# Performance work log

Measured on AMD Instinct MI355X. Metric: run time of the kernel, lower is better.

Reference implementation:

```python
import jax, jax.numpy as jnp
import numpy as np
from jax.ops import segment_sum

N_NODES = 100000
N_EDGES = 1600000
IN_DIM = 64
NUM_GRAPHS = 64
BN_EPS = 1e-5


def setup_inputs() -> dict:
    key = jax.random.key(0)
    ks = jax.random.split(key, 32)
    inp = {
        "x": jax.random.normal(ks[0], (N_NODES, IN_DIM), jnp.float32),
        "edge_index": jax.random.randint(ks[1], (2, N_EDGES), 0, N_NODES, jnp.int64),
        "edge_weight": jax.random.uniform(ks[2], (N_EDGES,), jnp.float32),
        "batch": jnp.sort(jax.random.randint(ks[3], (N_NODES,), 0, NUM_GRAPHS, jnp.int64)),
    }
    dims = [(IN_DIM, 32), (32, 64), (64, 128)]
    i = 4
    for li, (din, dout) in enumerate(dims, start=1):
        inp[f"w{li}"] = jax.random.normal(ks[i], (din, dout), jnp.float32) / np.sqrt(din); i += 1
        inp[f"b{li}"] = jax.random.normal(ks[i], (dout,), jnp.float32) * 0.01; i += 1
        inp[f"g{li}"] = 1.0 + 0.1 * jax.random.normal(ks[i], (dout,), jnp.float32); i += 1
        inp[f"be{li}"] = jax.random.normal(ks[i], (dout,), jnp.float32) * 0.01; i += 1
        inp[f"m{li}"] = jax.random.normal(ks[i], (dout,), jnp.float32) * 0.1; i += 1
        inp[f"v{li}"] = jax.random.uniform(ks[i], (dout,), jnp.float32) + 0.5; i += 1
    inp["fcw"] = jax.random.normal(ks[i], (128, 64), jnp.float32) / np.sqrt(128.0); i += 1
    inp["fcb"] = jax.random.normal(ks[i], (64,), jnp.float32) * 0.01; i += 1
    inp["ow"] = jax.random.normal(ks[i], (64, 1), jnp.float32) / 8.0; i += 1
    inp["ob"] = jax.random.normal(ks[i], (1,), jnp.float32) * 0.01
    return inp


def _gcn_norm(edge_index, edge_weight, n):
    # PyG GCNConv: add self-loops (weight 1), symmetric normalization.
    row, col = edge_index[0], edge_index[1]
    deg = segment_sum(edge_weight, col, num_segments=n) + 1.0  # +1 from self-loop
    dinv = jnp.where(deg > 0, 1.0 / jnp.sqrt(deg), 0.0)
    norm = dinv[row] * edge_weight * dinv[col]   # [E]
    self_norm = dinv * dinv                      # [N], self-loop coefficient
    return norm, self_norm


def _conv(x, w, b, row, col, norm, self_norm, n):
    h = x @ w                                                       # [N, dout]
    agg = segment_sum(h[row] * norm[:, None], col, num_segments=n)  # gather-scale-scatter
    return agg + self_norm[:, None] * h + b


def _bn_relu(x, g, be, m, v):
    # BatchNorm1d in eval mode (running stats), fused with ReLU. Dropout = identity (eval).
    return jax.nn.relu((x - m) * (g / jnp.sqrt(v + BN_EPS)) + be)


def reference(x, edge_index, edge_weight, batch,
              w1, b1, g1, be1, m1, v1,
              w2, b2, g2, be2, m2, v2,
              w3, b3, g3, be3, m3, v3,
              fcw, fcb, ow, ob):
    n = x.shape[0]
    row, col = edge_index[0], edge_index[1]
    norm, self_norm = _gcn_norm(edge_index, edge_weight, n)

    h = _bn_relu(_conv(x, w1, b1, row, col, norm, self_norm, n), g1, be1, m1, v1)
    h = _bn_relu(_conv(h, w2, b2, row, col, norm, self_norm, n), g2, be2, m2, v2)
    h = _bn_relu(_conv(h, w3, b3, row, col, norm, self_norm, n), g3, be3, m3, v3)

    # global mean pool over graphs
    sums = segment_sum(h, batch, num_segments=NUM_GRAPHS)                       # [G,128]
    cnts = segment_sum(jnp.ones((n,), h.dtype), batch, num_segments=NUM_GRAPHS)
    pooled = sums / jnp.maximum(cnts, 1.0)[:, None]

    h = jax.nn.relu(pooled @ fcw + fcb)
    return h @ ow + ob
```

## Files before the change

kernel.cpp:

```cpp
#include <hip/hip_runtime.h>
#include <math.h>

#define BN_EPS 1e-5f
#define NBSH 7
#define BKT 128

__device__ __forceinline__ float4 fma4(float s, float4 a, float4 b) {
    return make_float4(fmaf(s, a.x, b.x), fmaf(s, a.y, b.y),
                       fmaf(s, a.z, b.z), fmaf(s, a.w, b.w));
}
__device__ __forceinline__ float4 add4(float4 a, float4 b) {
    return make_float4(a.x + b.x, a.y + b.y, a.z + b.z, a.w + b.w);
}


__global__ __launch_bounds__(256) void chist_k(const int* __restrict__ ei,
                                               int* __restrict__ chist, int E, int NB) {
    __shared__ int h[1024];
    int t = threadIdx.x;
    for (int i = t; i < NB; i += 256) h[i] = 0;
    __syncthreads();
    for (int e = blockIdx.x * 256 + t; e < E; e += gridDim.x * 256)
        atomicAdd(&h[((unsigned)ei[E + e]) >> NBSH], 1);
    __syncthreads();
    for (int i = t; i < NB; i += 256) if (h[i]) atomicAdd(&chist[i], h[i]);
}

__global__ __launch_bounds__(1024) void cscan_k(const int* __restrict__ chist,
                                                int* __restrict__ cbase,
                                                int* __restrict__ ccur,
                                                int NB, int* __restrict__ rptrN, int E) {
    __shared__ int s[1024];
    int t = threadIdx.x;
    int v = (t < NB) ? chist[t] : 0;
    s[t] = v;
    __syncthreads();
    for (int off = 1; off < 1024; off <<= 1) {
        int x = (t >= off) ? s[t - off] : 0;
        __syncthreads();
        s[t] += x;
        __syncthreads();
    }
    int excl = s[t] - v;
    if (t < NB) { cbase[t] = excl; ccur[t] = excl; }
    if (t == 0) { cbase[NB] = E; rptrN[0] = E; }
}

__global__ __launch_bounds__(256) void cscat_k(const int* __restrict__ ei,
                                               const float* __restrict__ ew,
                                               int* __restrict__ ccur,
                                               int2* __restrict__ pairs0, int E, int NB) {
    __shared__ int h[1024];
    __shared__ int base[1024];
    int t = threadIdx.x;
    int CH = (E + gridDim.x - 1) / gridDim.x;
    int lo = blockIdx.x * CH;
    int hi = lo + CH < E ? lo + CH : E;

    for (int i = t; i < NB; i += 256) h[i] = 0;
    __syncthreads();
    for (int e = lo + t; e < hi; e += 256)
        atomicAdd(&h[((unsigned)ei[E + e]) >> NBSH], 1);
    __syncthreads();
    for (int i = t; i < NB; i += 256) {
        int c = h[i];
        base[i] = c ? atomicAdd(&ccur[i], c) : 0;
        h[i] = 0;
    }
    __syncthreads();
    for (int e = lo + t; e < hi; e += 256) {
        int c = ei[E + e];
        int b = ((unsigned)c) >> NBSH;
        int idx = base[b] + atomicAdd(&h[b], 1);
        pairs0[idx] = make_int2(ei[e] | ((c & (BKT - 1)) << 17), __float_as_int(ew[e]));
    }
}

__global__ __launch_bounds__(BKT) void fineA_k(const int2* __restrict__ pairs0,
                                               const int* __restrict__ cbase,
                                               int* __restrict__ rptr,
                                               float* __restrict__ dinv, int N) {
    int b = blockIdx.x;
    __shared__ int cnt[BKT];
    __shared__ float wsum[BKT];
    __shared__ int sc[BKT];
    int t = threadIdx.x;
    cnt[t] = 0; wsum[t] = 0.f;
    __syncthreads();
    int s = cbase[b], e = cbase[b + 1];
    for (int i = s + t; i < e; i += BKT) {
        int2 p = pairs0[i];
        int cib = ((unsigned)p.x) >> 17;
        atomicAdd(&cnt[cib], 1);
        atomicAdd(&wsum[cib], __int_as_float(p.y));
    }
    __syncthreads();
    int v = cnt[t];
    sc[t] = v;
    __syncthreads();
    for (int off = 1; off < BKT; off <<= 1) {
        int x = (t >= off) ? sc[t - off] : 0;
        __syncthreads();
        sc[t] += x;
        __syncthreads();
    }
    int node = b * BKT + t;
    if (node < N) {
        rptr[node] = s + sc[t] - v;
        dinv[node] = 1.0f / sqrtf(wsum[t] + 1.0f);
    }
}

__global__ __launch_bounds__(BKT) void fineB_k(const int2* __restrict__ pairs0,
                                               const int* __restrict__ cbase,
                                               const int* __restrict__ rptr,
                                               const float* __restrict__ dinv,
                                               int2* __restrict__ pairs, int N) {
    int b = blockIdx.x;
    __shared__ int cur[BKT];
    __shared__ float dc[BKT];
    int t = threadIdx.x;
    int node = b * BKT + t;
    cur[t] = (node < N) ? rptr[node] : 0;
    dc[t] = (node < N) ? dinv[node] : 0.f;
    __syncthreads();
    int s = cbase[b], e = cbase[b + 1];
    for (int i = s + t; i < e; i += BKT) {
        int2 p = pairs0[i];
        int cib = ((unsigned)p.x) >> 17;
        int row = p.x & 0x1FFFF;
        float nw = dinv[row] * __int_as_float(p.y) * dc[cib];
        int pos = atomicAdd(&cur[cib], 1);
        pairs[pos] = make_int2(row, __float_as_int(nw));
    }
}

template <int DIN, int DOUT>
__global__ __launch_bounds__(256) void matmul_k(const float* __restrict__ x,
                                                const float* __restrict__ w,
                                                float* __restrict__ h, int n) {
    constexpr int RPB = 64;
    constexpr int XS = DIN + 4;
    constexpr int J = DOUT / 16;
    __shared__ float xs[RPB * XS];
    __shared__ float4 ws4[DIN * (DOUT / 4)];
    int t = threadIdx.x;
    int row0 = blockIdx.x * RPB;

    for (int i = t; i < DIN * DOUT / 4; i += 256) ws4[i] = ((const float4*)w)[i];
    for (int i = t; i < RPB * DIN / 4; i += 256) {
        int r = i / (DIN / 4), kq = i % (DIN / 4);
        int gr = row0 + r;
        float4 xv = (gr < n) ? ((const float4*)x)[(size_t)gr * (DIN / 4) + kq]
                             : make_float4(0.f, 0.f, 0.f, 0.f);
        *(float4*)&xs[r * XS + kq * 4] = xv;
    }
    __syncthreads();

    int r = t >> 2, cg = t & 3;
    float4 acc[J];
#pragma unroll
    for (int j = 0; j < J; ++j) acc[j] = make_float4(0.f, 0.f, 0.f, 0.f);

    for (int k = 0; k < DIN; ++k) {
        float xv = xs[r * XS + k];
#pragma unroll
        for (int j = 0; j < J; ++j) {
            float4 wv = ws4[k * (DOUT / 4) + cg + 4 * j];
            acc[j] = fma4(xv, wv, acc[j]);
        }
    }
    int gr = row0 + r;
    if (gr < n) {
#pragma unroll
        for (int j = 0; j < J; ++j)
            ((float4*)h)[(size_t)gr * (DOUT / 4) + cg + 4 * j] = acc[j];
    }
}

template <int DIN, int DOUT>
__global__ __launch_bounds__(256) void matmulBN_k(const float* __restrict__ x,
                                                  const float* __restrict__ w,
                                                  const float* __restrict__ bias,
                                                  const float* __restrict__ g,
                                                  const float* __restrict__ be,
                                                  const float* __restrict__ m,
                                                  const float* __restrict__ v,
                                                  float* __restrict__ h, int n) {
    constexpr int RPB = 64;
    constexpr int XS = DIN + 4;
    constexpr int J = DOUT / 16;
    __shared__ float xs[RPB * XS];
    __shared__ float4 ws4[DIN * (DOUT / 4)];
    int t = threadIdx.x;
    int row0 = blockIdx.x * RPB;

    for (int i = t; i < DIN * DOUT / 4; i += 256) ws4[i] = ((const float4*)w)[i];
    for (int i = t; i < RPB * DIN / 4; i += 256) {
        int r = i / (DIN / 4), kq = i % (DIN / 4);
        int gr = row0 + r;
        float4 xv = (gr < n) ? ((const float4*)x)[(size_t)gr * (DIN / 4) + kq]
                             : make_float4(0.f, 0.f, 0.f, 0.f);
        *(float4*)&xs[r * XS + kq * 4] = xv;
    }
    __syncthreads();

    int r = t >> 2, cg = t & 3;
    float4 acc[J];
#pragma unroll
    for (int j = 0; j < J; ++j) acc[j] = make_float4(0.f, 0.f, 0.f, 0.f);

    for (int k = 0; k < DIN; ++k) {
        float xv = xs[r * XS + k];
#pragma unroll
        for (int j = 0; j < J; ++j) {
            float4 wv = ws4[k * (DOUT / 4) + cg + 4 * j];
            acc[j] = fma4(xv, wv, acc[j]);
        }
    }
    int gr = row0 + r;
    if (gr < n) {
#pragma unroll
        for (int j = 0; j < J; ++j) {
            int c4 = cg + 4 * j;
            float4 bb = ((const float4*)bias)[c4];
            float4 gg = ((const float4*)g)[c4];
            float4 ee = ((const float4*)be)[c4];
            float4 mm = ((const float4*)m)[c4];
            float4 vv = ((const float4*)v)[c4];
            float4 o = acc[j];
            float4 res;
            res.x = fmaxf((o.x + bb.x - mm.x) * (gg.x / sqrtf(vv.x + BN_EPS)) + ee.x, 0.f);
            res.y = fmaxf((o.y + bb.y - mm.y) * (gg.y / sqrtf(vv.y + BN_EPS)) + ee.y, 0.f);
            res.z = fmaxf((o.z + bb.z - mm.z) * (gg.z / sqrtf(vv.z + BN_EPS)) + ee.z, 0.f);
            res.w = fmaxf((o.w + bb.w - mm.w) * (gg.w / sqrtf(vv.w + BN_EPS)) + ee.w, 0.f);
            ((float4*)h)[(size_t)gr * (DOUT / 4) + c4] = res;
        }
    }
}

template <int TPN>
__device__ __forceinline__ float4 gather4(const float* __restrict__ h,
                                          const int2* __restrict__ pairs,
                                          int s, int e, int lc) {
    float4 a0 = make_float4(0.f, 0.f, 0.f, 0.f);
    float4 a1 = a0, a2 = a0, a3 = a0;
    int i = s;
    for (; i + 4 <= e; i += 4) {
        int2 p0 = pairs[i + 0];
        int2 p1 = pairs[i + 1];
        int2 p2 = pairs[i + 2];
        int2 p3 = pairs[i + 3];
        float4 h0 = ((const float4*)h)[(size_t)p0.x * TPN + lc];
        float4 h1 = ((const float4*)h)[(size_t)p1.x * TPN + lc];
        float4 h2 = ((const float4*)h)[(size_t)p2.x * TPN + lc];
        float4 h3 = ((const float4*)h)[(size_t)p3.x * TPN + lc];
        a0 = fma4(__int_as_float(p0.y), h0, a0);
        a1 = fma4(__int_as_float(p1.y), h1, a1);
        a2 = fma4(__int_as_float(p2.y), h2, a2);
        a3 = fma4(__int_as_float(p3.y), h3, a3);
    }
    for (; i < e; ++i) {
        int2 p = pairs[i];
        float4 hv = ((const float4*)h)[(size_t)p.x * TPN + lc];
        a0 = fma4(__int_as_float(p.y), hv, a0);
    }
    return add4(add4(a0, a1), add4(a2, a3));
}

template <int D>
__global__ __launch_bounds__(256) void agg_k(const float* __restrict__ h,
                                             const int* __restrict__ rptr,
                                             const int2* __restrict__ pairs,
                                             const float* __restrict__ dinv,
                                             const float* __restrict__ bias,
                                             const float* __restrict__ g,
                                             const float* __restrict__ be,
                                             const float* __restrict__ m,
                                             const float* __restrict__ v,
                                             float* __restrict__ y, int n) {
    constexpr int TPN = D / 4;
    int npb = 256 / TPN;
    int node = blockIdx.x * npb + (int)(threadIdx.x / TPN);
    int lc = (int)(threadIdx.x % TPN);
    if (node >= n) return;

    int s = rptr[node], e = rptr[node + 1];
    float4 acc = gather4<TPN>(h, pairs, s, e, lc);

    float dv = dinv[node];
    float sn = dv * dv;
    float4 hs = ((const float4*)h)[(size_t)node * TPN + lc];
    float4 bb = ((const float4*)bias)[lc];
    float4 gg = ((const float4*)g)[lc];
    float4 ee = ((const float4*)be)[lc];
    float4 mm = ((const float4*)m)[lc];
    float4 vv = ((const float4*)v)[lc];

    float4 o;
    o.x = acc.x + sn * hs.x + bb.x;
    o.y = acc.y + sn * hs.y + bb.y;
    o.z = acc.z + sn * hs.z + bb.z;
    o.w = acc.w + sn * hs.w + bb.w;

    float4 res;
    res.x = fmaxf((o.x - mm.x) * (gg.x / sqrtf(vv.x + BN_EPS)) + ee.x, 0.f);
    res.y = fmaxf((o.y - mm.y) * (gg.y / sqrtf(vv.y + BN_EPS)) + ee.y, 0.f);
    res.z = fmaxf((o.z - mm.z) * (gg.z / sqrtf(vv.z + BN_EPS)) + ee.z, 0.f);
    res.w = fmaxf((o.w - mm.w) * (gg.w / sqrtf(vv.w + BN_EPS)) + ee.w, 0.f);

    ((float4*)y)[(size_t)node * TPN + lc] = res;
}

template <int D>
__global__ __launch_bounds__(256) void aggpre_k(const float* __restrict__ h,
                                                const int* __restrict__ rptr,
                                                const int2* __restrict__ pairs,
                                                const float* __restrict__ dinv,
                                                float* __restrict__ z, int n) {
    constexpr int TPN = D / 4;
    int npb = 256 / TPN;
    int node = blockIdx.x * npb + (int)(threadIdx.x / TPN);
    int lc = (int)(threadIdx.x % TPN);
    if (node >= n) return;

    int s = rptr[node], e = rptr[node + 1];
    float4 acc = gather4<TPN>(h, pairs, s, e, lc);

    float dv = dinv[node];
    float sn = dv * dv;
    float4 hs = ((const float4*)h)[(size_t)node * TPN + lc];
    acc.x = fmaf(sn, hs.x, acc.x);
    acc.y = fmaf(sn, hs.y, acc.y);
    acc.z = fmaf(sn, hs.z, acc.z);
    acc.w = fmaf(sn, hs.w, acc.w);
    ((float4*)z)[(size_t)node * TPN + lc] = acc;
}

__global__ __launch_bounds__(256) void pool2_k(const float* __restrict__ y,
                                               const int* __restrict__ batch,
                                               float* __restrict__ sums, int n) {
    const int NPB = 256;
    int node0 = blockIdx.x * NPB;
    int lc = threadIdx.x & 31;
    int nr = threadIdx.x >> 5;
    int end = node0 + NPB < n ? node0 + NPB : n;

    float4 acc = make_float4(0.f, 0.f, 0.f, 0.f);
    int curg = -1;
    for (int i = node0 + nr; i < end; i += 8) {
        int gph = batch[i];
        if (gph != curg) {
            if (curg >= 0) {
                float* dst = &sums[curg * 128 + lc * 4];
                atomicAdd(dst + 0, acc.x);
                atomicAdd(dst + 1, acc.y);
                atomicAdd(dst + 2, acc.z);
                atomicAdd(dst + 3, acc.w);
            }
            acc = make_float4(0.f, 0.f, 0.f, 0.f);
            curg = gph;
        }
        float4 hv = ((const float4*)y)[(size_t)i * 32 + lc];
        acc.x += hv.x; acc.y += hv.y; acc.z += hv.z; acc.w += hv.w;
    }
    if (curg >= 0) {
        float* dst = &sums[curg * 128 + lc * 4];
        atomicAdd(dst + 0, acc.x);
        atomicAdd(dst + 1, acc.y);
        atomicAdd(dst + 2, acc.z);
        atomicAdd(dst + 3, acc.w);
    }
}

__global__ void gcnt_k(const int* __restrict__ batch, float* __restrict__ rcnt, int n) {
    int gph = threadIdx.x;
    if (gph >= 64) return;
    int lo = 0, hi = n;
    while (lo < hi) { int mid = (lo + hi) >> 1; if (batch[mid] < gph) lo = mid + 1; else hi = mid; }
    int s = lo;
    lo = 0; hi = n;
    while (lo < hi) { int mid = (lo + hi) >> 1; if (batch[mid] < gph + 1) lo = mid + 1; else hi = mid; }
    int c = lo - s;
    rcnt[gph] = 1.0f / (c > 0 ? (float)c : 1.0f);
}

__global__ __launch_bounds__(256) void fc_k(const float* __restrict__ sums,
                                            const float* __restrict__ rcnt,
                                            const float* __restrict__ fcw,
                                            const float* __restrict__ fcb,
                                            const float* __restrict__ ow,
                                            const float* __restrict__ ob,
                                            float* __restrict__ out) {
    __shared__ float ps[64 * 128];
    __shared__ float hs[64 * 64];
    int t = threadIdx.x;
    for (int i = t; i < 64 * 128; i += 256) ps[i] = sums[i] * rcnt[i >> 7];
    __syncthreads();
    for (int idx = t; idx < 64 * 64; idx += 256) {
        int gph = idx >> 6, j = idx & 63;
        float a = fcb[j];
        for (int k = 0; k < 128; ++k) a = fmaf(ps[gph * 128 + k], fcw[k * 64 + j], a);
        hs[idx] = fmaxf(a, 0.f);
    }
    __syncthreads();
    if (t < 64) {
        float a = ob[0];
        for (int j = 0; j < 64; ++j) a = fmaf(hs[t * 64 + j], ow[j], a);
        out[t] = a;
    }
}

extern "C" void kernel_launch(void* const* d_in, const int* in_sizes, int n_in,
                              void* d_out, int out_size, void* d_ws, size_t ws_size,
                              hipStream_t stream) {
    const float* x     = (const float*)d_in[0];
    const int*   ei    = (const int*)d_in[1];
    const float* ew    = (const float*)d_in[2];
    const int*   batch = (const int*)d_in[3];
    const float* w1 = (const float*)d_in[4],  *b1 = (const float*)d_in[5];
    const float* g1 = (const float*)d_in[6],  *be1 = (const float*)d_in[7];
    const float* m1 = (const float*)d_in[8],  *v1 = (const float*)d_in[9];
    const float* w2 = (const float*)d_in[10], *b2 = (const float*)d_in[11];
    const float* g2 = (const float*)d_in[12], *be2 = (const float*)d_in[13];
    const float* m2 = (const float*)d_in[14], *v2 = (const float*)d_in[15];
    const float* w3 = (const float*)d_in[16], *b3 = (const float*)d_in[17];
    const float* g3 = (const float*)d_in[18], *be3 = (const float*)d_in[19];
    const float* m3 = (const float*)d_in[20], *v3 = (const float*)d_in[21];
    const float* fcw = (const float*)d_in[22], *fcb = (const float*)d_in[23];
    const float* ow  = (const float*)d_in[24], *ob  = (const float*)d_in[25];
    float* out = (float*)d_out;

    const int N = in_sizes[3];
    const int E = in_sizes[2];
    const int NB = (N + BKT - 1) >> NBSH;

    float* A    = (float*)d_ws;
    float* Bf   = A + (size_t)N * 128;
    float* dinv = Bf + (size_t)N * 128;
    int*   rptr  = (int*)(dinv + N);
    int*   chist = rptr + (N + 1);
    int*   cbase = chist + NB;
    int*   ccur  = cbase + NB + 1;
    int2*  pairs = (int2*)(ccur + NB);
    float* sums  = (float*)(pairs + E);
    float* rcnt  = sums + 64 * 128;
    int2*  pairs0 = (int2*)A;

    hipMemsetAsync(chist, 0, NB * sizeof(int), stream);
    hipMemsetAsync(sums, 0, 64 * 128 * sizeof(float), stream);

    chist_k<<<256, 256, 0, stream>>>(ei, chist, E, NB);
    cscan_k<<<1, 1024, 0, stream>>>(chist, cbase, ccur, NB, rptr + N, E);
    cscat_k<<<256, 256, 0, stream>>>(ei, ew, ccur, pairs0, E, NB);
    fineA_k<<<NB, BKT, 0, stream>>>(pairs0, cbase, rptr, dinv, N);
    fineB_k<<<NB, BKT, 0, stream>>>(pairs0, cbase, rptr, dinv, pairs, N);

    matmul_k<64, 32><<<(N + 63) / 64, 256, 0, stream>>>(x, w1, A, N);
    agg_k<32><<<(N + 31) / 32, 256, 0, stream>>>(A, rptr, pairs, dinv,
                                                 b1, g1, be1, m1, v1, Bf, N);
    aggpre_k<32><<<(N + 31) / 32, 256, 0, stream>>>(Bf, rptr, pairs, dinv, A, N);
    matmulBN_k<32, 64><<<(N + 63) / 64, 256, 0, stream>>>(A, w2, b2, g2, be2, m2, v2, Bf, N);
    aggpre_k<64><<<(N + 15) / 16, 256, 0, stream>>>(Bf, rptr, pairs, dinv, A, N);
    matmulBN_k<64, 128><<<(N + 63) / 64, 256, 0, stream>>>(A, w3, b3, g3, be3, m3, v3, Bf, N);

    pool2_k<<<(N + 255) / 256, 256, 0, stream>>>(Bf, batch, sums, N);
    gcnt_k<<<1, 64, 0, stream>>>(batch, rcnt, N);
    fc_k<<<1, 256, 0, stream>>>(sums, rcnt, fcw, fcb, ow, ob, out);
}
```

Measured before the change: 366.0 us.

## Sub-sort CSR edges by source-row range within each destination node

The fine scatter kernel now does a counting sort of each bucket's edges keyed by destination node and source-row range (32 ranges of 4096 rows). Before, edges were placed per destination in arbitrary atomic order. Grouping by source row should improve cache locality of the gathers in the later aggregation kernels. The cost is an extra pass over the bucket, a shared-memory histogram and a block-wide scan in the one-time CSR build.

```diff
diff --git a/kernel.cpp b/kernel.cpp
--- a/kernel.cpp
+++ b/kernel.cpp
@@ -4,6 +4,8 @@
 #define BN_EPS 1e-5f
 #define NBSH 7
 #define BKT 128
+#define RTSH 12
+#define NT 32
 
 __device__ __forceinline__ float4 fma4(float s, float4 a, float4 b) {
     return make_float4(fmaf(s, a.x, b.x), fmaf(s, a.y, b.y),
@@ -111,26 +113,53 @@
     }
 }
 
-__global__ __launch_bounds__(BKT) void fineB_k(const int2* __restrict__ pairs0,
+__global__ __launch_bounds__(256) void fineB_k(const int2* __restrict__ pairs0,
                                                const int* __restrict__ cbase,
-                                               const int* __restrict__ rptr,
                                                const float* __restrict__ dinv,
                                                int2* __restrict__ pairs, int N) {
     int b = blockIdx.x;
-    __shared__ int cur[BKT];
+    __shared__ int bins[BKT * NT];
+    __shared__ int part[256];
     __shared__ float dc[BKT];
     int t = threadIdx.x;
-    int node = b * BKT + t;
-    cur[t] = (node < N) ? rptr[node] : 0;
-    dc[t] = (node < N) ? dinv[node] : 0.f;
+    for (int i = t; i < BKT * NT; i += 256) bins[i] = 0;
+    if (t < BKT) {
+        int node = b * BKT + t;
+        dc[t] = (node < N) ? dinv[node] : 0.f;
+    }
     __syncthreads();
     int s = cbase[b], e = cbase[b + 1];
-    for (int i = s + t; i < e; i += BKT) {
+    for (int i = s + t; i < e; i += 256) {
+        int px = pairs0[i].x;
+        int cib = ((unsigned)px) >> 17;
+        int row = px & 0x1FFFF;
+        atomicAdd(&bins[cib * NT + (((unsigned)row) >> RTSH)], 1);
+    }
+    __syncthreads();
+    int base = t * 16;
+    int loc[16];
+    int sum = 0;
+#pragma unroll
+    for (int j = 0; j < 16; ++j) { loc[j] = sum; sum += bins[base + j]; }
+    part[t] = sum;
+    __syncthreads();
+    for (int off = 1; off < 256; off <<= 1) {
+        int x = (t >= off) ? part[t - off] : 0;
+        __syncthreads();
+        part[t] += x;
+        __syncthreads();
+    }
+    int excl = part[t] - sum;
+    __syncthreads();
+#pragma unroll
+    for (int j = 0; j < 16; ++j) bins[base + j] = s + excl + loc[j];
+    __syncthreads();
+    for (int i = s + t; i < e; i += 256) {
         int2 p = pairs0[i];
         int cib = ((unsigned)p.x) >> 17;
         int row = p.x & 0x1FFFF;
         float nw = dinv[row] * __int_as_float(p.y) * dc[cib];
-        int pos = atomicAdd(&cur[cib], 1);
+        int pos = atomicAdd(&bins[cib * NT + (((unsigned)row) >> RTSH)], 1);
         pairs[pos] = make_int2(row, __float_as_int(nw));
     }
 }
@@ -454,7 +483,7 @@
     cscan_k<<<1, 1024, 0, stream>>>(chist, cbase, ccur, NB, rptr + N, E);
     cscat_k<<<256, 256, 0, stream>>>(ei, ew, ccur, pairs0, E, NB);
     fineA_k<<<NB, BKT, 0, stream>>>(pairs0, cbase, rptr, dinv, N);
-    fineB_k<<<NB, BKT, 0, stream>>>(pairs0, cbase, rptr, dinv, pairs, N);
+    fineB_k<<<NB, 256, 0, stream>>>(pairs0, cbase, dinv, pairs, N);
 
     matmul_k<64, 32><<<(N + 63) / 64, 256, 0, stream>>>(x, w1, A, N);
     agg_k<32><<<(N + 31) / 32, 256, 0, stream>>>(A, rptr, pairs, dinv,
```

Result: no change. 366.7 us (+0.2%).

## Fuse CSR fine-sort passes, defer row dinv to gather, merge memsets and gcnt

Applied to the files above, without the earlier changes.

Merges the two fine bucket passes into one kernel that stages the bucket's pairs in shared memory, so pairs0 is read from global memory once. The row-side dinv factor is no longer folded into the stored edge weight; each gather now multiplies by dinv[row] itself. gcnt is folded into fc_k and the two memsets become one by placing sums next to chist. This saves launches and one pass over the pairs, but adds a random dinv load per edge in every aggregation, which are the heaviest kernels.

```diff
diff --git a/kernel.cpp b/kernel.cpp
--- a/kernel.cpp
+++ b/kernel.cpp
@@ -4,6 +4,7 @@
 #define BN_EPS 1e-5f
 #define NBSH 7
 #define BKT 128
+#define CAP 3072
 
 __device__ __forceinline__ float4 fma4(float s, float4 a, float4 b) {
     return make_float4(fmaf(s, a.x, b.x), fmaf(s, a.y, b.y),
@@ -76,60 +77,56 @@
     }
 }
 
-__global__ __launch_bounds__(BKT) void fineA_k(const int2* __restrict__ pairs0,
-                                               const int* __restrict__ cbase,
-                                               int* __restrict__ rptr,
-                                               float* __restrict__ dinv, int N) {
+__global__ __launch_bounds__(256) void fineAB_k(const int2* __restrict__ pairs0,
+                                                const int* __restrict__ cbase,
+                                                int* __restrict__ rptr,
+                                                float* __restrict__ dinv,
+                                                int2* __restrict__ pairs, int N) {
     int b = blockIdx.x;
+    __shared__ int2 lp[CAP];
     __shared__ int cnt[BKT];
     __shared__ float wsum[BKT];
-    __shared__ int sc[BKT];
-    int t = threadIdx.x;
-    cnt[t] = 0; wsum[t] = 0.f;
+    __shared__ int sc[256];
+    __shared__ float dc[BKT];
+    __shared__ int cur[BKT];
+    int t = threadIdx.x;
+    if (t < BKT) { cnt[t] = 0; wsum[t] = 0.f; }
     __syncthreads();
     int s = cbase[b], e = cbase[b + 1];
-    for (int i = s + t; i < e; i += BKT) {
-        int2 p = pairs0[i];
+    int len = e - s;
+    int m = len < CAP ? len : CAP;
+    for (int i = t; i < m; i += 256) lp[i] = pairs0[s + i];
+    __syncthreads();
+    for (int i = t; i < len; i += 256) {
+        int2 p = (i < m) ? lp[i] : pairs0[s + i];
         int cib = ((unsigned)p.x) >> 17;
         atomicAdd(&cnt[cib], 1);
         atomicAdd(&wsum[cib], __int_as_float(p.y));
     }
     __syncthreads();
-    int v = cnt[t];
+    int v = (t < BKT) ? cnt[t] : 0;
     sc[t] = v;
     __syncthreads();
-    for (int off = 1; off < BKT; off <<= 1) {
+    for (int off = 1; off < 256; off <<= 1) {
         int x = (t >= off) ? sc[t - off] : 0;
         __syncthreads();
         sc[t] += x;
         __syncthreads();
     }
-    int node = b * BKT + t;
-    if (node < N) {
-        rptr[node] = s + sc[t] - v;
-        dinv[node] = 1.0f / sqrtf(wsum[t] + 1.0f);
-    }
-}
-
-__global__ __launch_bounds__(BKT) void fineB_k(const int2* __restrict__ pairs0,
-                                               const int* __restrict__ cbase,
-                                               const int* __restrict__ rptr,
-                                               const float* __restrict__ dinv,
-                                               int2* __restrict__ pairs, int N) {
-    int b = blockIdx.x;
-    __shared__ int cur[BKT];
-    __shared__ float dc[BKT];
-    int t = threadIdx.x;
-    int node = b * BKT + t;
-    cur[t] = (node < N) ? rptr[node] : 0;
-    dc[t] = (node < N) ? dinv[node] : 0.f;
-    __syncthreads();
-    int s = cbase[b], e = cbase[b + 1];
-    for (int i = s + t; i < e; i += BKT) {
-        int2 p = pairs0[i];
+    int excl = sc[t] - v;
+    if (t < BKT) {
+        int node = b * BKT + t;
+        cur[t] = s + excl;
+        float dv = 1.0f / sqrtf(wsum[t] + 1.0f);
+        dc[t] = dv;
+        if (node < N) { rptr[node] = s + excl; dinv[node] = dv; }
+    }
+    __syncthreads();
+    for (int i = t; i < len; i += 256) {
+        int2 p = (i < m) ? lp[i] : pairs0[s + i];
         int cib = ((unsigned)p.x) >> 17;
         int row = p.x & 0x1FFFF;
-        float nw = dinv[row] * __int_as_float(p.y) * dc[cib];
+        float nw = __int_as_float(p.y) * dc[cib];
         int pos = atomicAdd(&cur[cib], 1);
         pairs[pos] = make_int2(row, __float_as_int(nw));
     }
@@ -242,7 +239,9 @@
 template <int TPN>
 __device__ __forceinline__ float4 gather4(const float* __restrict__ h,
                                           const int2* __restrict__ pairs,
+                                          const float* __restrict__ dinv,
                                           int s, int e, int lc) {
+    const float4* __restrict__ hb = (const float4*)h;
     float4 a0 = make_float4(0.f, 0.f, 0.f, 0.f);
     float4 a1 = a0, a2 = a0, a3 = a0;
     int i = s;
@@ -251,19 +250,19 @@
         int2 p1 = pairs[i + 1];
         int2 p2 = pairs[i + 2];
         int2 p3 = pairs[i + 3];
-        float4 h0 = ((const float4*)h)[(size_t)p0.x * TPN + lc];
-        float4 h1 = ((const float4*)h)[(size_t)p1.x * TPN + lc];
-        float4 h2 = ((const float4*)h)[(size_t)p2.x * TPN + lc];
-        float4 h3 = ((const float4*)h)[(size_t)p3.x * TPN + lc];
-        a0 = fma4(__int_as_float(p0.y), h0, a0);
-        a1 = fma4(__int_as_float(p1.y), h1, a1);
-        a2 = fma4(__int_as_float(p2.y), h2, a2);
-        a3 = fma4(__int_as_float(p3.y), h3, a3);
+        float4 h0 = hb[(size_t)p0.x * TPN + lc];
+        float4 h1 = hb[(size_t)p1.x * TPN + lc];
+        float4 h2 = hb[(size_t)p2.x * TPN + lc];
+        float4 h3 = hb[(size_t)p3.x * TPN + lc];
+        a0 = fma4(__int_as_float(p0.y) * dinv[p0.x], h0, a0);
+        a1 = fma4(__int_as_float(p1.y) * dinv[p1.x], h1, a1);
+        a2 = fma4(__int_as_float(p2.y) * dinv[p2.x], h2, a2);
+        a3 = fma4(__int_as_float(p3.y) * dinv[p3.x], h3, a3);
     }
     for (; i < e; ++i) {
         int2 p = pairs[i];
-        float4 hv = ((const float4*)h)[(size_t)p.x * TPN + lc];
-        a0 = fma4(__int_as_float(p.y), hv, a0);
+        float4 hv = hb[(size_t)p.x * TPN + lc];
+        a0 = fma4(__int_as_float(p.y) * dinv[p.x], hv, a0);
     }
     return add4(add4(a0, a1), add4(a2, a3));
 }
@@ -286,7 +285,7 @@
     if (node >= n) return;
 
     int s = rptr[node], e = rptr[node + 1];
-    float4 acc = gather4<TPN>(h, pairs, s, e, lc);
+    float4 acc = gather4<TPN>(h, pairs, dinv, s, e, lc);
 
     float dv = dinv[node];
     float sn = dv * dv;
@@ -325,7 +324,7 @@
     if (node >= n) return;
 
     int s = rptr[node], e = rptr[node + 1];
-    float4 acc = gather4<TPN>(h, pairs, s, e, lc);
+    float4 acc = gather4<TPN>(h, pairs, dinv, s, e, lc);
 
     float dv = dinv[node];
     float sn = dv * dv;
@@ -373,20 +372,8 @@
     }
 }
 
-__global__ void gcnt_k(const int* __restrict__ batch, float* __restrict__ rcnt, int n) {
-    int gph = threadIdx.x;
-    if (gph >= 64) return;
-    int lo = 0, hi = n;
-    while (lo < hi) { int mid = (lo + hi) >> 1; if (batch[mid] < gph) lo = mid + 1; else hi = mid; }
-    int s = lo;
-    lo = 0; hi = n;
-    while (lo < hi) { int mid = (lo + hi) >> 1; if (batch[mid] < gph + 1) lo = mid + 1; else hi = mid; }
-    int c = lo - s;
-    rcnt[gph] = 1.0f / (c > 0 ? (float)c : 1.0f);
-}
-
 __global__ __launch_bounds__(256) void fc_k(const float* __restrict__ sums,
-                                            const float* __restrict__ rcnt,
+                                            const int* __restrict__ batch, int n,
                                             const float* __restrict__ fcw,
                                             const float* __restrict__ fcb,
                                             const float* __restrict__ ow,
@@ -394,8 +381,20 @@
                                             float* __restrict__ out) {
     __shared__ float ps[64 * 128];
     __shared__ float hs[64 * 64];
-    int t = threadIdx.x;
-    for (int i = t; i < 64 * 128; i += 256) ps[i] = sums[i] * rcnt[i >> 7];
+    __shared__ float rc[64];
+    int t = threadIdx.x;
+    if (t < 64) {
+        int gph = t;
+        int lo = 0, hi = n;
+        while (lo < hi) { int mid = (lo + hi) >> 1; if (batch[mid] < gph) lo = mid + 1; else hi = mid; }
+        int s0 = lo;
+        lo = 0; hi = n;
+        while (lo < hi) { int mid = (lo + hi) >> 1; if (batch[mid] < gph + 1) lo = mid + 1; else hi = mid; }
+        int c = lo - s0;
+        rc[t] = 1.0f / (c > 0 ? (float)c : 1.0f);
+    }
+    __syncthreads();
+    for (int i = t; i < 64 * 128; i += 256) ps[i] = sums[i] * rc[i >> 7];
     __syncthreads();
     for (int idx = t; idx < 64 * 64; idx += 256) {
         int gph = idx >> 6, j = idx & 63;
@@ -440,21 +439,18 @@
     float* dinv = Bf + (size_t)N * 128;
     int*   rptr  = (int*)(dinv + N);
     int*   chist = rptr + (N + 1);
-    int*   cbase = chist + NB;
+    float* sums  = (float*)(chist + NB);
+    int*   cbase = (int*)(sums + 64 * 128);
     int*   ccur  = cbase + NB + 1;
     int2*  pairs = (int2*)(ccur + NB);
-    float* sums  = (float*)(pairs + E);
-    float* rcnt  = sums + 64 * 128;
     int2*  pairs0 = (int2*)A;
 
-    hipMemsetAsync(chist, 0, NB * sizeof(int), stream);
-    hipMemsetAsync(sums, 0, 64 * 128 * sizeof(float), stream);
+    hipMemsetAsync(chist, 0, (NB + 64 * 128) * sizeof(int), stream);
 
     chist_k<<<256, 256, 0, stream>>>(ei, chist, E, NB);
     cscan_k<<<1, 1024, 0, stream>>>(chist, cbase, ccur, NB, rptr + N, E);
     cscat_k<<<256, 256, 0, stream>>>(ei, ew, ccur, pairs0, E, NB);
-    fineA_k<<<NB, BKT, 0, stream>>>(pairs0, cbase, rptr, dinv, N);
-    fineB_k<<<NB, BKT, 0, stream>>>(pairs0, cbase, rptr, dinv, pairs, N);
+    fineAB_k<<<NB, 256, 0, stream>>>(pairs0, cbase, rptr, dinv, pairs, N);
 
     matmul_k<64, 32><<<(N + 63) / 64, 256, 0, stream>>>(x, w1, A, N);
     agg_k<32><<<(N + 31) / 32, 256, 0, stream>>>(A, rptr, pairs, dinv,
@@ -465,6 +461,5 @@
     matmulBN_k<64, 128><<<(N + 63) / 64, 256, 0, stream>>>(A, w3, b3, g3, be3, m3, v3, Bf, N);
 
     pool2_k<<<(N + 255) / 256, 256, 0, stream>>>(Bf, batch, sums, N);
-    gcnt_k<<<1, 64, 0, stream>>>(batch, rcnt, N);
-    fc_k<<<1, 256, 0, stream>>>(sums, rcnt, fcw, fcb, ow, ob, out);
-}
+    fc_k<<<1, 256, 0, stream>>>(sums, batch, N, fcw, fcb, ow, ob, out);
+}
```

Result: faster. 357.8 us (-2.2%).
